# Kernel tuning notes

Hardware: AMD Instinct MI355X
Metric: run time of the kernel (lower is better)

Reference implementation:

```python
import jax, jax.numpy as jnp
import numpy as np

T, B, E, H = 2048, 2, 2048, 16
D = E // H  # 128


def setup_inputs() -> dict:
    key = jax.random.key(0)
    ks = jax.random.split(key, 4)
    query = jax.random.normal(ks[0], (T, B, E), dtype=jnp.float32)
    Wqkv = jax.random.normal(ks[1], (3 * E, E), dtype=jnp.float32) * 0.02
    bqkv = jnp.zeros((3 * E,), dtype=jnp.float32)
    Wo = jax.random.normal(ks[2], (E, E), dtype=jnp.float32) * 0.02
    bo = jnp.zeros((E,), dtype=jnp.float32)
    # Llama rotary frequencies: freqs_cis[t, j] = exp(i * t * theta^{-2j/D})
    inv_freq = 1.0 / (10000.0 ** (np.arange(0, D, 2, dtype=np.float32) / D))  # (D/2,)
    angles = np.arange(T, dtype=np.float32)[:, None] * inv_freq[None, :]       # (T, D/2)
    freqs_cos = jnp.asarray(np.cos(angles), dtype=jnp.float32)
    freqs_sin = jnp.asarray(np.sin(angles), dtype=jnp.float32)
    return {"query": query, "Wqkv": Wqkv, "bqkv": bqkv, "Wo": Wo, "bo": bo,
            "freqs_cos": freqs_cos, "freqs_sin": freqs_sin}


def _apply_rope(x, cos, sin):
    # Faithful to metaseq: x is (T, B, E) but view()-ed as (B, T, H, D);
    # jnp.reshape is the same row-major reinterpretation as torch .view().
    xr = x.reshape(B, T, H, D // 2, 2)
    x0, x1 = xr[..., 0], xr[..., 1]
    c = cos[None, :, None, :]  # broadcast over batch and heads, seq_dim=1
    s = sin[None, :, None, :]
    o0 = x0 * c - x1 * s
    o1 = x0 * s + x1 * c
    return jnp.stack([o0, o1], axis=-1).reshape(T, B, E)


def reference(query, Wqkv, bqkv, Wo, bo, freqs_cos, freqs_sin):
    # Combined QKV projection (ColumnParallelLinear, world_size=1), split order (k, v, q)
    kvq = jnp.einsum('tbe,fe->tbf', query, Wqkv) + bqkv  # (T, B, 3E)
    k, v, q = jnp.split(kvq, 3, axis=-1)
    q = _apply_rope(q, freqs_cos, freqs_sin)
    k = _apply_rope(k, freqs_cos, freqs_sin)
    # scaling split as sqrt(head_dim^-0.5) on both q and k (baddbmm path)
    s = jnp.asarray(D, jnp.float32) ** -0.25
    qb = q.reshape(T, B * H, D).swapaxes(0, 1) * s   # (BH, T, D)
    kb = k.reshape(T, B * H, D).swapaxes(0, 1) * s   # (BH, S, D)
    vb = v.reshape(T, B * H, D).swapaxes(0, 1)       # (BH, S, D)
    scores = jnp.einsum('btd,bsd->bts', qb, kb)      # (BH, T, S)
    causal = jnp.tril(jnp.ones((T, T), dtype=bool))  # ScaledUpperTriangMaskedSoftmax
    scores = jnp.where(causal[None, :, :], scores, jnp.finfo(scores.dtype).min)
    probs = jax.nn.softmax(scores, axis=-1)          # dropout p=0 -> identity
    attn = jnp.einsum('bts,bsd->btd', probs, vb)     # (BH, T, D)
    attn = attn.swapaxes(0, 1).reshape(T, B, E)
    # RowParallelLinear with skip_bias_add=True: bias returned separately (not added)
    out = jnp.einsum('tbe,fe->tbf', attn, Wo)
    return out
```

## Files before the change

### kernel.cpp

```cpp
#include <hip/hip_runtime.h>
#include <stdint.h>

typedef unsigned short u16;
typedef __attribute__((ext_vector_type(4))) float f32x4;
typedef __attribute__((ext_vector_type(8))) short bf16x8;
typedef __attribute__((ext_vector_type(8))) u16 u16x8;

#define T_SEQ  2048
#define EMB    2048
#define HD     128
#define NHEAD  16
#define NTOK   4096
#define NE3    6144
#define SCALE  0.29730177875068026f
#define LOG2E  1.44269504088896f

typedef __attribute__((address_space(3))) char* lds_t;
typedef const __attribute__((address_space(1))) char* gl_t;

__device__ __forceinline__ void gld16(const void* g, void* l) {
  __builtin_amdgcn_global_load_lds((gl_t)g, (lds_t)l, 16, 0, 0);
}

__device__ __forceinline__ u16 f2bf(float f) {
  union { float f; uint32_t u; } c; c.f = f;
  uint32_t r = c.u + 0x7fffu + ((c.u >> 16) & 1u);
  return (u16)(r >> 16);
}

__global__ __launch_bounds__(256) void cvt_bf16(const float* __restrict__ in,
                                                u16* __restrict__ out, int n8) {
  int i = blockIdx.x * 256 + threadIdx.x;
  if (i >= n8) return;
  const float4* p = (const float4*)in + (size_t)i * 2;
  float4 a = p[0], b = p[1];
  u16x8 o;
  o[0]=f2bf(a.x); o[1]=f2bf(a.y); o[2]=f2bf(a.z); o[3]=f2bf(a.w);
  o[4]=f2bf(b.x); o[5]=f2bf(b.y); o[6]=f2bf(b.z); o[7]=f2bf(b.w);
  *((u16x8*)out + i) = o;
}

__device__ __forceinline__ bf16x8 rdfrag(const char* slot, int row, int lq) {
  return *(const bf16x8*)(slot + row*64 + ((lq ^ ((row >> 1) & 3)) << 4));
}
__device__ __forceinline__ void stg512(const char* g, int K2, int kbyte,
                                       char* slot, int j, int tid) {
  int lb = j*8192 + tid*16;
  int row = lb >> 6, c = (lb >> 4) & 3;
  gld16(g + (size_t)row*K2 + kbyte + ((c ^ ((row >> 1) & 3)) << 4), slot + lb);
}

template<int EPI>
__global__ __launch_bounds__(512, 2) void gemmF(
    const u16* __restrict__ A, const u16* __restrict__ Bm, int K, int N,
    const float* __restrict__ cosT, const float* __restrict__ sinT,
    const float* __restrict__ bias,
    u16* __restrict__ Qh, u16* __restrict__ Kh, u16* __restrict__ Vt,
    float* __restrict__ Cout)
{
  __shared__ __align__(16) char lds[98304];
  const int tid = threadIdx.x;
  const int lane = tid & 63, w = tid >> 6;
  const int wm = w >> 2, wn = w & 3;
  const int l15 = lane & 15, lq = lane >> 4;

  const int i = blockIdx.x;
  const int r = i >> 8, x = i & 7, s = (i >> 3) & 31;
  const int regionId = r*8 + x;
  const int bM = (regionId & 3)*8 + (s >> 2);
  const int bN = (regionId >> 2)*4 + (s & 3);

  const char* Ag = (const char*)(A + (size_t)bM * 128 * K);
  const char* Bg = (const char*)(Bm + (size_t)bN * 256 * K);
  const int K2 = K * 2;
  const int nT = K >> 5;

  #define BUF(k) (lds + ((k) & 3) * 24576)
  #define STAGE(t) do { int kb_ = (t) << 6; char* b_ = BUF(t);        \
    stg512(Ag, K2, kb_, b_, 0, tid);                                  \
    stg512(Bg, K2, kb_, b_ + 8192, 0, tid);                           \
    stg512(Bg, K2, kb_, b_ + 8192, 1, tid); } while (0)

  STAGE(0); STAGE(1); STAGE(2);
  asm volatile("s_waitcnt vmcnt(6)" ::: "memory");
  __builtin_amdgcn_s_barrier();
  __builtin_amdgcn_sched_barrier(0);

  bf16x8 afA[4], bfA[4], afB[4], bfB[4];
  #pragma unroll
  for (int j = 0; j < 4; j++) afA[j] = rdfrag(BUF(0), wm*64 + j*16 + l15, lq);
  #pragma unroll
  for (int j = 0; j < 4; j++) bfA[j] = rdfrag(BUF(0) + 8192, wn*64 + j*16 + l15, lq);

  f32x4 acc[4][4] = {};

  #define ITER(t, CA, CB, OA, OB) do {                                     \
    asm volatile("s_waitcnt vmcnt(3)" ::: "memory");  \
    __builtin_amdgcn_s_barrier();                                          \
    __builtin_amdgcn_sched_barrier(0);                                     \
    const int tr_ = ((t) + 1 < nT) ? (t) + 1 : nT - 1;                     \
    const char* rb_ = BUF(tr_);                                            \
    _Pragma("unroll")                                                      \
    for (int j_ = 0; j_ < 4; j_++) OA[j_] = rdfrag(rb_, wm*64 + j_*16 + l15, lq); \
    _Pragma("unroll")                                                      \
    for (int j_ = 0; j_ < 4; j_++) OB[j_] = rdfrag(rb_ + 8192, wn*64 + j_*16 + l15, lq); \
    asm volatile("s_waitcnt lgkmcnt(8)" ::: "memory");  \
    __builtin_amdgcn_sched_barrier(0);                                     \
    const int ts_ = ((t) + 3 < nT) ? (t) + 3 : nT - 1;                     \
    STAGE(ts_);                                                            \
    __builtin_amdgcn_s_setprio(1);                                         \
    _Pragma("unroll")                                                      \
    for (int mi_ = 0; mi_ < 4; mi_++)                                      \
      _Pragma("unroll")                                                    \
      for (int ni_ = 0; ni_ < 4; ni_++)                                    \
        acc[mi_][ni_] = __builtin_amdgcn_mfma_f32_16x16x32_bf16(CA[mi_], CB[ni_], acc[mi_][ni_], 0, 0, 0); \
    __builtin_amdgcn_s_setprio(0);                                         \
  } while (0)

  for (int t = 0; t < nT; t += 2) {
    ITER(t,     afA, bfA, afB, bfB);
    ITER(t + 1, afB, bfB, afA, bfA);
  }
  asm volatile("s_waitcnt vmcnt(0) lgkmcnt(0)" ::: "memory");
  __builtin_amdgcn_sched_barrier(0);
  #undef ITER
  #undef STAGE
  #undef BUF

  if (EPI == 0) {
    #pragma unroll
    for (int mi = 0; mi < 4; mi++) {
      int row = bM*128 + wm*64 + mi*16 + lq*4;
      #pragma unroll
      for (int ni = 0; ni < 4; ni++) {
        int col = bN*256 + wn*64 + ni*16 + l15;
        #pragma unroll
        for (int rr = 0; rr < 4; rr++)
          Cout[(size_t)(row + rr) * N + col] = acc[mi][ni][rr];
      }
    }
  } else {
    const int cbase = bN*256 + wn*64;
    const int seg  = cbase >> 11;
    const int head = (cbase >> 7) & 15;
    #pragma unroll
    for (int mi = 0; mi < 4; mi++) {
      #pragma unroll
      for (int ni = 0; ni < 4; ni++) {
        int col = cbase + ni*16 + l15;
        int d = col & 127;
        float bi = bias[col];
        f32x4 v = acc[mi][ni];
        #pragma unroll
        for (int rr = 0; rr < 4; rr++) {
          int n = bM*128 + wm*64 + mi*16 + lq*4 + rr;
          float val = v[rr] + bi;
          int t = n >> 1, b = n & 1;
          int bh = b*NHEAD + head;
          if (seg == 1) {
            Vt[((size_t)bh*HD + d)*T_SEQ + t] = f2bf(val);
          } else {
            float par = __shfl_xor(val, 1);
            int fidx = d >> 1;
            float cs = cosT[(n & (T_SEQ-1))*64 + fidx];
            float sn = sinT[(n & (T_SEQ-1))*64 + fidx];
            val = (d & 1) ? (par*sn + val*cs) : (val*cs - par*sn);
            val *= SCALE;
            u16* dst = (seg == 0) ? Kh : Qh;
            dst[((size_t)bh*T_SEQ + t)*HD + d] = f2bf(val);
          }
        }
      }
    }
  }
}

#define PSW(row) ((((row) & 7) << 4) ^ (((row) & 8) << 2))

__global__ __launch_bounds__(512, 4) void attn_fwd(
    const u16* __restrict__ Qh, const u16* __restrict__ Kh,
    const u16* __restrict__ Vt, u16* __restrict__ O)
{
  const int i = blockIdx.x;
  const int kk = i >> 8, c = i & 255;
  const int b5 = c & 15;
  const int qb = kk ? (15 - b5) : b5;
  const int bh = (c >> 4) + kk * 16;

  const int tid = threadIdx.x, lane = tid & 63, w = tid >> 6;
  const int l15 = lane & 15, lq = lane >> 4;

  __shared__ u16 Ks[2][64*128];
  __shared__ u16 Vs[2][128*64];
  __shared__ char Ps[8][2048];

  const int q0 = qb*128 + w*16;
  bf16x8 qf[4];
  #pragma unroll
  for (int dc = 0; dc < 4; dc++)
    qf[dc] = *(const bf16x8*)(Qh + ((size_t)bh*T_SEQ + q0 + l15)*HD + dc*32 + lq*8);

  const int nkb = 2*qb + 2;

  #define STAGE_KV(t, b) do {                                              \
    _Pragma("unroll")                                                      \
    for (int j_ = 0; j_ < 2; j_++) {                                       \
      int lb_ = tid*16 + j_*8192;                                          \
      int row_ = lb_ >> 8, bir_ = lb_ & 255;                               \
      int sb_ = bir_ ^ ((row_ & 7) << 4);                                  \
      gld16((const char*)Kh + (((size_t)bh*T_SEQ + (t)*64 + row_) << 8) + sb_, \
            (char*)Ks[b] + lb_);                                           \
    }                                                                      \
    _Pragma("unroll")                                                      \
    for (int j_ = 0; j_ < 2; j_++) {                                       \
      int lb_ = tid*16 + j_*8192;                                          \
      int row_ = lb_ >> 7, bir_ = lb_ & 127;                               \
      int sb_ = bir_ ^ ((row_ & 7) << 4);                                  \
      gld16((const char*)Vt + ((size_t)(bh*HD + row_)*T_SEQ)*2 + (t)*128 + sb_, \
            (char*)Vs[b] + lb_);                                           \
    }                                                                      \
  } while (0)

  STAGE_KV(0, 0);
  STAGE_KV(1, 1);

  f32x4 o[8] = {};
  float m[4], l_[4];
  #pragma unroll
  for (int r = 0; r < 4; r++) { m[r] = -1e30f; l_[r] = 0.f; }

  for (int kb = 0; kb < nkb; ++kb) {
    asm volatile("s_waitcnt vmcnt(4)" ::: "memory");
    __builtin_amdgcn_s_barrier();
    __builtin_amdgcn_sched_barrier(0);

    const char* Kb = (const char*)Ks[kb & 1];
    const char* Vb = (const char*)Vs[kb & 1];

    f32x4 sacc[4];
    #pragma unroll
    for (int nf = 0; nf < 4; nf++) {
      f32x4 z = {};
      sacc[nf] = z;
      #pragma unroll
      for (int dc = 0; dc < 4; dc++) {
        int row = nf*16 + l15;
        int bir = (dc*64 + lq*16) ^ ((row & 7) << 4);
        bf16x8 kf = *(const bf16x8*)(Kb + row*256 + bir);
        sacc[nf] = __builtin_amdgcn_mfma_f32_16x16x32_bf16(qf[dc], kf, sacc[nf], 0, 0, 0);
      }
    }

    if (kb*64 + 63 > q0) {
      #pragma unroll
      for (int nf = 0; nf < 4; nf++)
        #pragma unroll
        for (int r = 0; r < 4; r++) {
          int key = kb*64 + nf*16 + l15;
          int qr  = q0 + lq*4 + r;
          if (key > qr) sacc[nf][r] = -1e30f;
        }
    }

    #pragma unroll
    for (int r = 0; r < 4; r++) {
      float mx = fmaxf(fmaxf(sacc[0][r], sacc[1][r]), fmaxf(sacc[2][r], sacc[3][r]));
      mx = fmaxf(mx, __shfl_xor(mx, 1));
      mx = fmaxf(mx, __shfl_xor(mx, 2));
      mx = fmaxf(mx, __shfl_xor(mx, 4));
      mx = fmaxf(mx, __shfl_xor(mx, 8));
      float newm = fmaxf(m[r], mx);
      float scale = exp2f((m[r] - newm) * LOG2E);
      float sum = 0.f;
      #pragma unroll
      for (int nf = 0; nf < 4; nf++) {
        float p = exp2f((sacc[nf][r] - newm) * LOG2E);
        sacc[nf][r] = p;
        sum += p;
      }
      sum += __shfl_xor(sum, 1);
      sum += __shfl_xor(sum, 2);
      sum += __shfl_xor(sum, 4);
      sum += __shfl_xor(sum, 8);
      l_[r] = l_[r] * scale + sum;
      m[r] = newm;
      #pragma unroll
      for (int nf = 0; nf < 8; nf++) o[nf][r] *= scale;
    }

    #pragma unroll
    for (int nf = 0; nf < 4; nf++)
      #pragma unroll
      for (int r = 0; r < 4; r++) {
        int prow = lq*4 + r;
        int pbyte = prow*128 + (((nf*16 + l15)*2) ^ PSW(prow));
        *(u16*)(Ps[w] + pbyte) = f2bf(sacc[nf][r]);
      }

    #pragma unroll
    for (int kc = 0; kc < 2; kc++) {
      int pb = (kc*64 + lq*16) ^ PSW(l15);
      bf16x8 pf = *(const bf16x8*)(Ps[w] + l15*128 + pb);
      #pragma unroll
      for (int nf = 0; nf < 8; nf++) {
        int row = nf*16 + l15;
        int bir = (kc*64 + lq*16) ^ ((row & 7) << 4);
        bf16x8 vf = *(const bf16x8*)(Vb + row*128 + bir);
        o[nf] = __builtin_amdgcn_mfma_f32_16x16x32_bf16(pf, vf, o[nf], 0, 0, 0);
      }
    }

    __builtin_amdgcn_s_barrier();
    const int tnext = (kb + 2 < nkb) ? kb + 2 : nkb - 1;
    STAGE_KV(tnext, kb & 1);
  }
  asm volatile("s_waitcnt vmcnt(0)" ::: "memory");
  #undef STAGE_KV

  const int b = bh >> 4, h = bh & 15;
  #pragma unroll
  for (int r = 0; r < 4; r++) {
    float inv = 1.0f / l_[r];
    int t = q0 + lq*4 + r;
    size_t base = ((size_t)(t*2 + b))*EMB + h*HD;
    #pragma unroll
    for (int nf = 0; nf < 8; nf++)
      O[base + nf*16 + l15] = f2bf(o[nf][r] * inv);
  }
}

extern "C" void kernel_launch(void* const* d_in, const int* in_sizes, int n_in,
                              void* d_out, int out_size, void* d_ws, size_t ws_size,
                              hipStream_t stream) {
  const float* query = (const float*)d_in[0];
  const float* Wqkv  = (const float*)d_in[1];
  const float* bqkv  = (const float*)d_in[2];
  const float* Wo    = (const float*)d_in[3];
  const float* fcos  = (const float*)d_in[5];
  const float* fsin  = (const float*)d_in[6];
  float* out = (float*)d_out;
  char* ws = (char*)d_ws;

  u16* WQb = (u16*)(ws + 0);
  u16* WOb = (u16*)(ws + 25165824);
  u16* A1  = (u16*)(ws + 33554432);
  u16* QH  = (u16*)(ws + 50331648);
  u16* KH  = (u16*)(ws + 67108864);
  u16* VT  = (u16*)(ws + 83886080);

  cvt_bf16<<<4096, 256, 0, stream>>>(query, A1, 1048576);
  cvt_bf16<<<6144, 256, 0, stream>>>(Wqkv, WQb, 1572864);
  cvt_bf16<<<2048, 256, 0, stream>>>(Wo,   WOb,  524288);

  gemmF<1><<<768, 512, 0, stream>>>(A1, WQb, 2048, NE3,
                                    fcos, fsin, bqkv, QH, KH, VT, nullptr);

  attn_fwd<<<512, 512, 0, stream>>>(QH, KH, VT, A1);

  gemmF<0><<<256, 512, 0, stream>>>(A1, WOb, 2048, EMB,
                                    nullptr, nullptr, nullptr,
                                    nullptr, nullptr, nullptr, out);
}
```

Before: 315.3 us.

## Replace GEMM with 8-phase ping-pong pipeline and 256-row tiles for QKV

Rewrites the bf16 GEMM kernel as a two-buffer, eight-phase schedule with K-step 64. Global-to-LDS loads of A and B halves are interleaved with MFMA quarters, separated by barriers. LDS uses a 128-byte row swizzle, and the tile M size is now a template parameter: 256 rows for the QKV projection (384 blocks) and 128 for the output projection. The goal is better overlap of memory and matrix-core work and more reuse per loaded B tile. The cost is more LDS per block (up to 160KB), which may limit occupancy, and more barriers.

```diff
diff --git a/kernel.cpp b/kernel.cpp
--- a/kernel.cpp
+++ b/kernel.cpp
@@ -10,7 +10,6 @@
 #define EMB    2048
 #define HD     128
 #define NHEAD  16
-#define NTOK   4096
 #define NE3    6144
 #define SCALE  0.29730177875068026f
 #define LOG2E  1.44269504088896f
@@ -40,97 +39,137 @@
   *((u16x8*)out + i) = o;
 }
 
-__device__ __forceinline__ bf16x8 rdfrag(const char* slot, int row, int lq) {
-  return *(const bf16x8*)(slot + row*64 + ((lq ^ ((row >> 1) & 3)) << 4));
-}
-__device__ __forceinline__ void stg512(const char* g, int K2, int kbyte,
-                                       char* slot, int j, int tid) {
-  int lb = j*8192 + tid*16;
-  int row = lb >> 6, c = (lb >> 4) & 3;
-  gld16(g + (size_t)row*K2 + kbyte + ((c ^ ((row >> 1) & 3)) << 4), slot + lb);
-}
-
-template<int EPI>
-__global__ __launch_bounds__(512, 2) void gemmF(
+__device__ __forceinline__ bf16x8 frg(const char* m, int row, int ks, int lq) {
+  return *(const bf16x8*)(m + row*128 + ((ks*64 + lq*16) ^ ((row & 7) << 4)));
+}
+
+template<int EPI, int BM>
+__global__ __launch_bounds__(512, 2) void gemm8p(
     const u16* __restrict__ A, const u16* __restrict__ Bm, int K, int N,
     const float* __restrict__ cosT, const float* __restrict__ sinT,
     const float* __restrict__ bias,
     u16* __restrict__ Qh, u16* __restrict__ Kh, u16* __restrict__ Vt,
     float* __restrict__ Cout)
 {
-  __shared__ __align__(16) char lds[98304];
+  constexpr int ASLAB = BM * 128;
+  constexpr int MFR   = BM / 64;
+  constexpr int AHB   = ASLAB / 2;
+  constexpr int AHR   = AHB / 8192;
+  __shared__ __align__(16) char lds[2 * (ASLAB + 32768)];
+
   const int tid = threadIdx.x;
   const int lane = tid & 63, w = tid >> 6;
   const int wm = w >> 2, wn = w & 3;
   const int l15 = lane & 15, lq = lane >> 4;
 
-  const int i = blockIdx.x;
-  const int r = i >> 8, x = i & 7, s = (i >> 3) & 31;
-  const int regionId = r*8 + x;
-  const int bM = (regionId & 3)*8 + (s >> 2);
-  const int bN = (regionId >> 2)*4 + (s & 3);
-
-  const char* Ag = (const char*)(A + (size_t)bM * 128 * K);
+  constexpr int NBMd4 = (4096 / BM) / 4;
+  const int region = blockIdx.x >> 4, s = blockIdx.x & 15;
+  const int bM = (region % NBMd4) * 4 + (s >> 2);
+  const int bN = (region / NBMd4) * 4 + (s & 3);
+
+  const char* Ag = (const char*)(A + (size_t)bM * BM * K);
   const char* Bg = (const char*)(Bm + (size_t)bN * 256 * K);
   const int K2 = K * 2;
-  const int nT = K >> 5;
-
-  #define BUF(k) (lds + ((k) & 3) * 24576)
-  #define STAGE(t) do { int kb_ = (t) << 6; char* b_ = BUF(t);        \
-    stg512(Ag, K2, kb_, b_, 0, tid);                                  \
-    stg512(Bg, K2, kb_, b_ + 8192, 0, tid);                           \
-    stg512(Bg, K2, kb_, b_ + 8192, 1, tid); } while (0)
-
-  STAGE(0); STAGE(1); STAGE(2);
-  asm volatile("s_waitcnt vmcnt(6)" ::: "memory");
-  __builtin_amdgcn_s_barrier();
-  __builtin_amdgcn_sched_barrier(0);
-
-  bf16x8 afA[4], bfA[4], afB[4], bfB[4];
-  #pragma unroll
-  for (int j = 0; j < 4; j++) afA[j] = rdfrag(BUF(0), wm*64 + j*16 + l15, lq);
-  #pragma unroll
-  for (int j = 0; j < 4; j++) bfA[j] = rdfrag(BUF(0) + 8192, wn*64 + j*16 + l15, lq);
-
-  f32x4 acc[4][4] = {};
-
-  #define ITER(t, CA, CB, OA, OB) do {                                     \
-    asm volatile("s_waitcnt vmcnt(3)" ::: "memory");  \
-    __builtin_amdgcn_s_barrier();                                          \
-    __builtin_amdgcn_sched_barrier(0);                                     \
-    const int tr_ = ((t) + 1 < nT) ? (t) + 1 : nT - 1;                     \
-    const char* rb_ = BUF(tr_);                                            \
-    _Pragma("unroll")                                                      \
-    for (int j_ = 0; j_ < 4; j_++) OA[j_] = rdfrag(rb_, wm*64 + j_*16 + l15, lq); \
-    _Pragma("unroll")                                                      \
-    for (int j_ = 0; j_ < 4; j_++) OB[j_] = rdfrag(rb_ + 8192, wn*64 + j_*16 + l15, lq); \
-    asm volatile("s_waitcnt lgkmcnt(8)" ::: "memory");  \
-    __builtin_amdgcn_sched_barrier(0);                                     \
-    const int ts_ = ((t) + 3 < nT) ? (t) + 3 : nT - 1;                     \
-    STAGE(ts_);                                                            \
-    __builtin_amdgcn_s_setprio(1);                                         \
-    _Pragma("unroll")                                                      \
-    for (int mi_ = 0; mi_ < 4; mi_++)                                      \
-      _Pragma("unroll")                                                    \
-      for (int ni_ = 0; ni_ < 4; ni_++)                                    \
-        acc[mi_][ni_] = __builtin_amdgcn_mfma_f32_16x16x32_bf16(CA[mi_], CB[ni_], acc[mi_][ni_], 0, 0, 0); \
-    __builtin_amdgcn_s_setprio(0);                                         \
-  } while (0)
-
-  for (int t = 0; t < nT; t += 2) {
-    ITER(t,     afA, bfA, afB, bfB);
-    ITER(t + 1, afB, bfB, afA, bfA);
+  const int nT = K >> 6;
+
+  char* LA0 = lds;
+  char* LB0 = lds + ASLAB;
+  char* LA1 = lds + ASLAB + 32768;
+  char* LB1 = LA1 + ASLAB;
+
+  #define STG_A(t, h, LA) do {                                           \
+    _Pragma("unroll") for (int j_ = 0; j_ < AHR; ++j_) {                 \
+      int lb_ = j_*8192 + tid*16;                                        \
+      int row_ = (h)*(BM/2) + (lb_ >> 7);                                \
+      gld16(Ag + (size_t)row_*K2 + (t)*128 + ((lb_&127) ^ ((row_&7)<<4)),\
+            (LA) + (h)*AHB + lb_); } } while (0)
+  #define STG_B(t, h, LB) do {                                           \
+    _Pragma("unroll") for (int j_ = 0; j_ < 2; ++j_) {                   \
+      int lb_ = j_*8192 + tid*16;                                        \
+      int row_ = (h)*128 + (lb_ >> 7);                                   \
+      gld16(Bg + (size_t)row_*K2 + (t)*128 + ((lb_&127) ^ ((row_&7)<<4)),\
+            (LB) + (h)*16384 + lb_); } } while (0)
+  #define RD_A(LA, mq_) _Pragma("unroll") for (int mi_ = 0; mi_ < MFR; ++mi_) \
+    { _Pragma("unroll") for (int ks_ = 0; ks_ < 2; ++ks_)                     \
+      Ar[mi_][ks_] = frg(LA, wm*(BM/2) + (mq_)*(BM/4) + mi_*16 + l15, ks_, lq); }
+  #define RD_B(LB, nq_, Br) _Pragma("unroll") for (int ni_ = 0; ni_ < 2; ++ni_) \
+    { _Pragma("unroll") for (int ks_ = 0; ks_ < 2; ++ks_)                       \
+      Br[ni_][ks_] = frg(LB, wn*64 + (nq_)*32 + ni_*16 + l15, ks_, lq); }
+  #define MM(mq_, nq_, Br) do { __builtin_amdgcn_s_setprio(1);                \
+    _Pragma("unroll") for (int mi_ = 0; mi_ < MFR; ++mi_)                     \
+    _Pragma("unroll") for (int ni_ = 0; ni_ < 2; ++ni_)                       \
+    _Pragma("unroll") for (int ks_ = 0; ks_ < 2; ++ks_)                       \
+      acc[(mq_)*MFR+mi_][(nq_)*2+ni_] = __builtin_amdgcn_mfma_f32_16x16x32_bf16( \
+        Ar[mi_][ks_], Br[ni_][ks_], acc[(mq_)*MFR+mi_][(nq_)*2+ni_], 0,0,0);  \
+    __builtin_amdgcn_s_setprio(0); } while (0)
+  #define MIDBAR do { __builtin_amdgcn_s_barrier();                      \
+    asm volatile("s_waitcnt lgkmcnt(0)" ::: "memory");                   \
+    __builtin_amdgcn_sched_barrier(0); } while (0)
+  #define ENDBAR do { __builtin_amdgcn_s_barrier();                      \
+    __builtin_amdgcn_sched_barrier(0); } while (0)
+
+  STG_B(0, 0, LB0); STG_B(0, 1, LB0);
+  STG_A(0, 0, LA0); STG_A(0, 1, LA0);
+  STG_B(1, 0, LB1); STG_B(1, 1, LB1);
+  asm volatile("s_waitcnt vmcnt(4)" ::: "memory");
+  ENDBAR;
+
+  f32x4 acc[2*MFR][4] = {};
+  bf16x8 Ar[MFR][2], Br0[2][2], Br1[2][2];
+
+  for (int it = 0; it < nT/2; ++it) {
+    const int t0 = 2*it, t1 = t0 + 1;
+    const int tc0 = (t0 + 2 < nT) ? t0 + 2 : nT - 1;
+    const int tc1 = (t1 + 2 < nT) ? t1 + 2 : nT - 1;
+
+    RD_A(LA0, 0); RD_B(LB0, 0, Br0);
+    STG_A(t1, 0, LA1);
+    if (MFR == 4) asm volatile("s_waitcnt lgkmcnt(8)" ::: "memory");
+    MIDBAR;  MM(0, 0, Br0);  ENDBAR;
+    RD_B(LB0, 1, Br1);
+    STG_A(t1, 1, LA1);
+    MIDBAR;  MM(0, 1, Br1);  ENDBAR;
+    RD_A(LA0, 1);
+    STG_B(tc0, 0, LB0);
+    MIDBAR;  MM(1, 0, Br0);  ENDBAR;
+    STG_B(tc0, 1, LB0);
+    __builtin_amdgcn_s_barrier();
+    __builtin_amdgcn_sched_barrier(0);
+    MM(1, 1, Br1);
+    asm volatile("s_waitcnt vmcnt(4)" ::: "memory");
+    ENDBAR;
+
+    RD_A(LA1, 0); RD_B(LB1, 0, Br0);
+    STG_A(tc0, 0, LA0);
+    if (MFR == 4) asm volatile("s_waitcnt lgkmcnt(8)" ::: "memory");
+    MIDBAR;  MM(0, 0, Br0);  ENDBAR;
+    RD_B(LB1, 1, Br1);
+    STG_A(tc0, 1, LA0);
+    MIDBAR;  MM(0, 1, Br1);  ENDBAR;
+    RD_A(LA1, 1);
+    STG_B(tc1, 0, LB1);
+    MIDBAR;  MM(1, 0, Br0);  ENDBAR;
+    STG_B(tc1, 1, LB1);
+    __builtin_amdgcn_s_barrier();
+    __builtin_amdgcn_sched_barrier(0);
+    MM(1, 1, Br1);
+    asm volatile("s_waitcnt vmcnt(4)" ::: "memory");
+    ENDBAR;
   }
   asm volatile("s_waitcnt vmcnt(0) lgkmcnt(0)" ::: "memory");
   __builtin_amdgcn_sched_barrier(0);
-  #undef ITER
-  #undef STAGE
-  #undef BUF
+  #undef STG_A
+  #undef STG_B
+  #undef RD_A
+  #undef RD_B
+  #undef MM
+  #undef MIDBAR
+  #undef ENDBAR
 
   if (EPI == 0) {
     #pragma unroll
-    for (int mi = 0; mi < 4; mi++) {
-      int row = bM*128 + wm*64 + mi*16 + lq*4;
+    for (int mi = 0; mi < 2*MFR; mi++) {
+      int row = bM*BM + wm*(BM/2) + mi*16 + lq*4;
       #pragma unroll
       for (int ni = 0; ni < 4; ni++) {
         int col = bN*256 + wn*64 + ni*16 + l15;
@@ -144,7 +183,7 @@
     const int seg  = cbase >> 11;
     const int head = (cbase >> 7) & 15;
     #pragma unroll
-    for (int mi = 0; mi < 4; mi++) {
+    for (int mi = 0; mi < 2*MFR; mi++) {
       #pragma unroll
       for (int ni = 0; ni < 4; ni++) {
         int col = cbase + ni*16 + l15;
@@ -153,7 +192,7 @@
         f32x4 v = acc[mi][ni];
         #pragma unroll
         for (int rr = 0; rr < 4; rr++) {
-          int n = bM*128 + wm*64 + mi*16 + lq*4 + rr;
+          int n = bM*BM + wm*(BM/2) + mi*16 + lq*4 + rr;
           float val = v[rr] + bi;
           int t = n >> 1, b = n & 1;
           int bh = b*NHEAD + head;
@@ -352,12 +391,12 @@
   cvt_bf16<<<6144, 256, 0, stream>>>(Wqkv, WQb, 1572864);
   cvt_bf16<<<2048, 256, 0, stream>>>(Wo,   WOb,  524288);
 
-  gemmF<1><<<768, 512, 0, stream>>>(A1, WQb, 2048, NE3,
-                                    fcos, fsin, bqkv, QH, KH, VT, nullptr);
+  gemm8p<1, 256><<<384, 512, 0, stream>>>(A1, WQb, 2048, NE3,
+                                          fcos, fsin, bqkv, QH, KH, VT, nullptr);
 
   attn_fwd<<<512, 512, 0, stream>>>(QH, KH, VT, A1);
 
-  gemmF<0><<<256, 512, 0, stream>>>(A1, WOb, 2048, EMB,
-                                    nullptr, nullptr, nullptr,
-                                    nullptr, nullptr, nullptr, out);
-}
+  gemm8p<0, 128><<<256, 512, 0, stream>>>(A1, WOb, 2048, EMB,
+                                          nullptr, nullptr, nullptr,
+                                          nullptr, nullptr, nullptr, out);
+}
```

Result: slower. 333.0 us (+5.6%).

## Use a 256x384 tile, 1024-thread single-wave QKV GEMM with triple-buffered LDS

Applied to the files above, without the earlier changes.

Splits the templated GEMM into a dedicated QKV kernel and a separate output-projection kernel. The QKV kernel uses 256x384 tiles with 16 waves per block, so 256 blocks cover the whole 4096x6144 output in one wave instead of 768 smaller blocks. Staging uses a 3-slot LDS ring of 40 KB slots. The intent is more operand reuse per LDS byte, fewer redundant global loads, and no tail wave. The trade-off is losing the register double-buffered fragment prefetch: each step waits for all LDS reads before its MFMAs, and LDS use rises to 120 KB per block.

```diff
diff --git a/kernel.cpp b/kernel.cpp
--- a/kernel.cpp
+++ b/kernel.cpp
@@ -10,7 +10,6 @@
 #define EMB    2048
 #define HD     128
 #define NHEAD  16
-#define NTOK   4096
 #define NE3    6144
 #define SCALE  0.29730177875068026f
 #define LOG2E  1.44269504088896f
@@ -50,12 +49,112 @@
   gld16(g + (size_t)row*K2 + kbyte + ((c ^ ((row >> 1) & 3)) << 4), slot + lb);
 }
 
-template<int EPI>
-__global__ __launch_bounds__(512, 2) void gemmF(
-    const u16* __restrict__ A, const u16* __restrict__ Bm, int K, int N,
+__global__ __launch_bounds__(1024, 4) void gemmQ(
+    const u16* __restrict__ A, const u16* __restrict__ Bm, int K,
     const float* __restrict__ cosT, const float* __restrict__ sinT,
     const float* __restrict__ bias,
-    u16* __restrict__ Qh, u16* __restrict__ Kh, u16* __restrict__ Vt,
+    u16* __restrict__ Qh, u16* __restrict__ Kh, u16* __restrict__ Vt)
+{
+  __shared__ __align__(16) char lds[122880];
+  const int tid = threadIdx.x;
+  const int lane = tid & 63, w = tid >> 6;
+  const int wm = w >> 2, wn = w & 3;
+  const int l15 = lane & 15, lq = lane >> 4;
+
+  const int i = blockIdx.x;
+  const int x = i & 7, s = i >> 3;
+  const int bM = (x & 3) * 4 + (s >> 3);
+  const int bN = (x >> 2) * 8 + (s & 7);
+
+  const char* Ag = (const char*)(A + (size_t)bM * 256 * K);
+  const char* Bg = (const char*)(Bm + (size_t)bN * 384 * K);
+  const int K2 = K * 2;
+  const int nT = K >> 5;
+
+  #define SBUF(k) (lds + ((k) % 3) * 40960)
+  #define STAGEQ(tsrc, bufk) do {                                            \
+    char* b_ = SBUF(bufk);                                                   \
+    const int kb_ = (tsrc) << 6;                                             \
+    { int lb_ = tid*16; int r_ = lb_ >> 6; int c_ = (lb_ >> 4) & 3;          \
+      gld16(Ag + (size_t)r_*K2 + kb_ + ((c_ ^ ((r_>>1)&3)) << 4), b_ + lb_); } \
+    { int lb_ = tid*16; int r_ = lb_ >> 6; int c_ = (lb_ >> 4) & 3;          \
+      gld16(Bg + (size_t)r_*K2 + kb_ + ((c_ ^ ((r_>>1)&3)) << 4),            \
+            b_ + 16384 + lb_); }                                             \
+    { int lb_ = (tid & 511)*16; int r_ = 256 + (lb_ >> 6);                   \
+      int c_ = (lb_ >> 4) & 3;                                               \
+      gld16(Bg + (size_t)r_*K2 + kb_ + ((c_ ^ ((r_>>1)&3)) << 4),            \
+            b_ + 32768 + lb_); }                                             \
+  } while (0)
+
+  STAGEQ(0, 0);
+  STAGEQ(1, 1);
+
+  f32x4 acc[4][6] = {};
+
+  for (int t = 0; t < nT; ++t) {
+    asm volatile("s_waitcnt vmcnt(3)" ::: "memory");
+    __builtin_amdgcn_s_barrier();
+    __builtin_amdgcn_sched_barrier(0);
+
+    const char* Ab = SBUF(t);
+    const char* Bb = Ab + 16384;
+    const int tsrc = (t + 2 < nT) ? t + 2 : nT - 1;
+    STAGEQ(tsrc, t + 2);
+
+    bf16x8 af[4], bf[6];
+    #pragma unroll
+    for (int j = 0; j < 4; j++) af[j] = rdfrag(Ab, wm*64 + j*16 + l15, lq);
+    #pragma unroll
+    for (int j = 0; j < 6; j++) bf[j] = rdfrag(Bb, wn*96 + j*16 + l15, lq);
+    asm volatile("s_waitcnt lgkmcnt(0)" ::: "memory");
+    __builtin_amdgcn_sched_barrier(0);
+    __builtin_amdgcn_s_setprio(1);
+    #pragma unroll
+    for (int mi = 0; mi < 4; mi++)
+      #pragma unroll
+      for (int ni = 0; ni < 6; ni++)
+        acc[mi][ni] = __builtin_amdgcn_mfma_f32_16x16x32_bf16(af[mi], bf[ni], acc[mi][ni], 0, 0, 0);
+    __builtin_amdgcn_s_setprio(0);
+  }
+  asm volatile("s_waitcnt vmcnt(0)" ::: "memory");
+  #undef STAGEQ
+  #undef SBUF
+
+  #pragma unroll
+  for (int mi = 0; mi < 4; mi++) {
+    #pragma unroll
+    for (int ni = 0; ni < 6; ni++) {
+      const int col16 = bN*384 + wn*96 + ni*16;
+      const int seg  = col16 >> 11;
+      const int head = (col16 >> 7) & 15;
+      const int d = (col16 & 127) + l15;
+      float bi = bias[col16 + l15];
+      f32x4 v = acc[mi][ni];
+      #pragma unroll
+      for (int rr = 0; rr < 4; rr++) {
+        int n = bM*256 + wm*64 + mi*16 + lq*4 + rr;
+        float val = v[rr] + bi;
+        int t = n >> 1, b = n & 1;
+        int bh = b*NHEAD + head;
+        if (seg == 1) {
+          Vt[((size_t)bh*HD + d)*T_SEQ + t] = f2bf(val);
+        } else {
+          float par = __shfl_xor(val, 1);
+          int fidx = d >> 1;
+          float cs = cosT[(n & (T_SEQ-1))*64 + fidx];
+          float sn = sinT[(n & (T_SEQ-1))*64 + fidx];
+          val = (d & 1) ? (par*sn + val*cs) : (val*cs - par*sn);
+          val *= SCALE;
+          u16* dst = (seg == 0) ? Kh : Qh;
+          dst[((size_t)bh*T_SEQ + t)*HD + d] = f2bf(val);
+        }
+      }
+    }
+  }
+}
+
+__global__ __launch_bounds__(512, 2) void gemmO(
+    const u16* __restrict__ A, const u16* __restrict__ Bm, int K, int N,
     float* __restrict__ Cout)
 {
   __shared__ __align__(16) char lds[98304];
@@ -95,7 +194,7 @@
   f32x4 acc[4][4] = {};
 
   #define ITER(t, CA, CB, OA, OB) do {                                     \
-    asm volatile("s_waitcnt vmcnt(3)" ::: "memory");  \
+    asm volatile("s_waitcnt vmcnt(3)" ::: "memory");                       \
     __builtin_amdgcn_s_barrier();                                          \
     __builtin_amdgcn_sched_barrier(0);                                     \
     const int tr_ = ((t) + 1 < nT) ? (t) + 1 : nT - 1;                     \
@@ -104,7 +203,7 @@
     for (int j_ = 0; j_ < 4; j_++) OA[j_] = rdfrag(rb_, wm*64 + j_*16 + l15, lq); \
     _Pragma("unroll")                                                      \
     for (int j_ = 0; j_ < 4; j_++) OB[j_] = rdfrag(rb_ + 8192, wn*64 + j_*16 + l15, lq); \
-    asm volatile("s_waitcnt lgkmcnt(8)" ::: "memory");  \
+    asm volatile("s_waitcnt lgkmcnt(8)" ::: "memory");                     \
     __builtin_amdgcn_sched_barrier(0);                                     \
     const int ts_ = ((t) + 3 < nT) ? (t) + 3 : nT - 1;                     \
     STAGE(ts_);                                                            \
@@ -127,50 +226,15 @@
   #undef STAGE
   #undef BUF
 
-  if (EPI == 0) {
-    #pragma unroll
-    for (int mi = 0; mi < 4; mi++) {
-      int row = bM*128 + wm*64 + mi*16 + lq*4;
-      #pragma unroll
-      for (int ni = 0; ni < 4; ni++) {
-        int col = bN*256 + wn*64 + ni*16 + l15;
-        #pragma unroll
-        for (int rr = 0; rr < 4; rr++)
-          Cout[(size_t)(row + rr) * N + col] = acc[mi][ni][rr];
-      }
-    }
-  } else {
-    const int cbase = bN*256 + wn*64;
-    const int seg  = cbase >> 11;
-    const int head = (cbase >> 7) & 15;
-    #pragma unroll
-    for (int mi = 0; mi < 4; mi++) {
-      #pragma unroll
-      for (int ni = 0; ni < 4; ni++) {
-        int col = cbase + ni*16 + l15;
-        int d = col & 127;
-        float bi = bias[col];
-        f32x4 v = acc[mi][ni];
-        #pragma unroll
-        for (int rr = 0; rr < 4; rr++) {
-          int n = bM*128 + wm*64 + mi*16 + lq*4 + rr;
-          float val = v[rr] + bi;
-          int t = n >> 1, b = n & 1;
-          int bh = b*NHEAD + head;
-          if (seg == 1) {
-            Vt[((size_t)bh*HD + d)*T_SEQ + t] = f2bf(val);
-          } else {
-            float par = __shfl_xor(val, 1);
-            int fidx = d >> 1;
-            float cs = cosT[(n & (T_SEQ-1))*64 + fidx];
-            float sn = sinT[(n & (T_SEQ-1))*64 + fidx];
-            val = (d & 1) ? (par*sn + val*cs) : (val*cs - par*sn);
-            val *= SCALE;
-            u16* dst = (seg == 0) ? Kh : Qh;
-            dst[((size_t)bh*T_SEQ + t)*HD + d] = f2bf(val);
-          }
-        }
-      }
+  #pragma unroll
+  for (int mi = 0; mi < 4; mi++) {
+    int row = bM*128 + wm*64 + mi*16 + lq*4;
+    #pragma unroll
+    for (int ni = 0; ni < 4; ni++) {
+      int col = bN*256 + wn*64 + ni*16 + l15;
+      #pragma unroll
+      for (int rr = 0; rr < 4; rr++)
+        Cout[(size_t)(row + rr) * N + col] = acc[mi][ni][rr];
     }
   }
 }
@@ -352,12 +416,10 @@
   cvt_bf16<<<6144, 256, 0, stream>>>(Wqkv, WQb, 1572864);
   cvt_bf16<<<2048, 256, 0, stream>>>(Wo,   WOb,  524288);
 
-  gemmF<1><<<768, 512, 0, stream>>>(A1, WQb, 2048, NE3,
-                                    fcos, fsin, bqkv, QH, KH, VT, nullptr);
+  gemmQ<<<256, 1024, 0, stream>>>(A1, WQb, 2048,
+                                  fcos, fsin, bqkv, QH, KH, VT);
 
   attn_fwd<<<512, 512, 0, stream>>>(QH, KH, VT, A1);
 
-  gemmF<0><<<256, 512, 0, stream>>>(A1, WOb, 2048, EMB,
-                                    nullptr, nullptr, nullptr,
-                                    nullptr, nullptr, nullptr, out);
-}
+  gemmO<<<256, 512, 0, stream>>>(A1, WOb, 2048, EMB, out);
+}
```

New measurement: 616.4 us. 1.95x slower.

## Shrink GEMM pipeline to three LDS stages and drop register double-buffering

Applied to the files above, without the earlier changes.

Cuts the GEMM's LDS ring from four 24 KB stages to three and raises the launch-bounds occupancy hint from 2 to 4 blocks per CU. The fragment prefetch into a second register set is removed: each iteration now issues the next global stage, reads its own fragments and waits for all LDS reads before the MFMAs. The goal is higher occupancy so other wavefronts hide latency instead of explicit software pipelining. In exchange, LDS read latency is exposed within each wave, prefetch depth is shallower, and the tighter register budget may cause spills. Reusing a buffer one iteration after it is read also relies on the per-iteration barrier for correctness.

```diff
diff --git a/kernel.cpp b/kernel.cpp
--- a/kernel.cpp
+++ b/kernel.cpp
@@ -10,7 +10,6 @@
 #define EMB    2048
 #define HD     128
 #define NHEAD  16
-#define NTOK   4096
 #define NE3    6144
 #define SCALE  0.29730177875068026f
 #define LOG2E  1.44269504088896f
@@ -51,14 +50,14 @@
 }
 
 template<int EPI>
-__global__ __launch_bounds__(512, 2) void gemmF(
+__global__ __launch_bounds__(512, 4) void gemmF(
     const u16* __restrict__ A, const u16* __restrict__ Bm, int K, int N,
     const float* __restrict__ cosT, const float* __restrict__ sinT,
     const float* __restrict__ bias,
     u16* __restrict__ Qh, u16* __restrict__ Kh, u16* __restrict__ Vt,
     float* __restrict__ Cout)
 {
-  __shared__ __align__(16) char lds[98304];
+  __shared__ __align__(16) char lds[73728];
   const int tid = threadIdx.x;
   const int lane = tid & 63, w = tid >> 6;
   const int wm = w >> 2, wn = w & 3;
@@ -75,55 +74,41 @@
   const int K2 = K * 2;
   const int nT = K >> 5;
 
-  #define BUF(k) (lds + ((k) & 3) * 24576)
+  #define BUF(k) (lds + ((k) % 3) * 24576)
   #define STAGE(t) do { int kb_ = (t) << 6; char* b_ = BUF(t);        \
     stg512(Ag, K2, kb_, b_, 0, tid);                                  \
     stg512(Bg, K2, kb_, b_ + 8192, 0, tid);                           \
     stg512(Bg, K2, kb_, b_ + 8192, 1, tid); } while (0)
 
-  STAGE(0); STAGE(1); STAGE(2);
-  asm volatile("s_waitcnt vmcnt(6)" ::: "memory");
-  __builtin_amdgcn_s_barrier();
-  __builtin_amdgcn_sched_barrier(0);
-
-  bf16x8 afA[4], bfA[4], afB[4], bfB[4];
-  #pragma unroll
-  for (int j = 0; j < 4; j++) afA[j] = rdfrag(BUF(0), wm*64 + j*16 + l15, lq);
-  #pragma unroll
-  for (int j = 0; j < 4; j++) bfA[j] = rdfrag(BUF(0) + 8192, wn*64 + j*16 + l15, lq);
+  STAGE(0); STAGE(1);
 
   f32x4 acc[4][4] = {};
 
-  #define ITER(t, CA, CB, OA, OB) do {                                     \
-    asm volatile("s_waitcnt vmcnt(3)" ::: "memory");  \
-    __builtin_amdgcn_s_barrier();                                          \
-    __builtin_amdgcn_sched_barrier(0);                                     \
-    const int tr_ = ((t) + 1 < nT) ? (t) + 1 : nT - 1;                     \
-    const char* rb_ = BUF(tr_);                                            \
-    _Pragma("unroll")                                                      \
-    for (int j_ = 0; j_ < 4; j_++) OA[j_] = rdfrag(rb_, wm*64 + j_*16 + l15, lq); \
-    _Pragma("unroll")                                                      \
-    for (int j_ = 0; j_ < 4; j_++) OB[j_] = rdfrag(rb_ + 8192, wn*64 + j_*16 + l15, lq); \
-    asm volatile("s_waitcnt lgkmcnt(8)" ::: "memory");  \
-    __builtin_amdgcn_sched_barrier(0);                                     \
-    const int ts_ = ((t) + 3 < nT) ? (t) + 3 : nT - 1;                     \
-    STAGE(ts_);                                                            \
-    __builtin_amdgcn_s_setprio(1);                                         \
-    _Pragma("unroll")                                                      \
-    for (int mi_ = 0; mi_ < 4; mi_++)                                      \
-      _Pragma("unroll")                                                    \
-      for (int ni_ = 0; ni_ < 4; ni_++)                                    \
-        acc[mi_][ni_] = __builtin_amdgcn_mfma_f32_16x16x32_bf16(CA[mi_], CB[ni_], acc[mi_][ni_], 0, 0, 0); \
-    __builtin_amdgcn_s_setprio(0);                                         \
-  } while (0)
-
-  for (int t = 0; t < nT; t += 2) {
-    ITER(t,     afA, bfA, afB, bfB);
-    ITER(t + 1, afB, bfB, afA, bfA);
+  for (int t = 0; t < nT; ++t) {
+    asm volatile("s_waitcnt vmcnt(3)" ::: "memory");
+    __builtin_amdgcn_s_barrier();
+    __builtin_amdgcn_sched_barrier(0);
+
+    const int ts = (t + 2 < nT) ? t + 2 : nT - 1;
+    STAGE(ts);
+
+    const char* rb = BUF(t);
+    bf16x8 af[4], bf[4];
+    #pragma unroll
+    for (int j = 0; j < 4; j++) af[j] = rdfrag(rb, wm*64 + j*16 + l15, lq);
+    #pragma unroll
+    for (int j = 0; j < 4; j++) bf[j] = rdfrag(rb + 8192, wn*64 + j*16 + l15, lq);
+    asm volatile("s_waitcnt lgkmcnt(0)" ::: "memory");
+    __builtin_amdgcn_sched_barrier(0);
+    __builtin_amdgcn_s_setprio(1);
+    #pragma unroll
+    for (int mi = 0; mi < 4; mi++)
+      #pragma unroll
+      for (int ni = 0; ni < 4; ni++)
+        acc[mi][ni] = __builtin_amdgcn_mfma_f32_16x16x32_bf16(af[mi], bf[ni], acc[mi][ni], 0, 0, 0);
+    __builtin_amdgcn_s_setprio(0);
   }
-  asm volatile("s_waitcnt vmcnt(0) lgkmcnt(0)" ::: "memory");
-  __builtin_amdgcn_sched_barrier(0);
-  #undef ITER
+  asm volatile("s_waitcnt vmcnt(0)" ::: "memory");
   #undef STAGE
   #undef BUF
 
```

After: 326.4 us. +3.5%, slower.
